# Optimization experiments

Measured on AMD Instinct MI355X. Metric: run time of the kernel, lower is better.

The kernel has to match this reference:

```python
import jax, jax.numpy as jnp
import numpy as np
from jax import lax

SUBSTEPS = 10
MACRO_DT = 1.0
MICRO_DT = MACRO_DT / float(SUBSTEPS)
MAX_DAYS = 4  # matches fill_max of delta_t_days; inactive batch items are masked to zero update


def _laplacian3d(u):
    # u: [B, 1, D, H, W]; 6-point stencil with zero (Dirichlet) padding at the boundary
    up = jnp.pad(u, ((0, 0), (0, 0), (1, 1), (1, 1), (1, 1)))
    return (up[:, :, 2:, 1:-1, 1:-1] + up[:, :, :-2, 1:-1, 1:-1]
            + up[:, :, 1:-1, 2:, 1:-1] + up[:, :, 1:-1, :-2, 1:-1]
            + up[:, :, 1:-1, 1:-1, 2:] + up[:, :, 1:-1, 1:-1, :-2]
            - 6.0 * u)


def _fisher_kolmogorov(u, D_map, rho_map):
    # du/dt = D * laplacian(u) + rho * u * (1 - u)
    return D_map * _laplacian3d(u) + rho_map * u * (1.0 - u)


def setup_inputs() -> dict:
    key = jax.random.key(0)
    k1, k2, k3, k4 = jax.random.split(key, 4)
    shape = (2, 1, 128, 128, 128)
    u_t0 = jax.random.uniform(k1, shape, dtype=jnp.float32)
    D_map = jax.random.uniform(k2, shape, dtype=jnp.float32) * 0.1   # diffusion, keep CFL-stable
    rho_map = jax.random.uniform(k3, shape, dtype=jnp.float32) * 0.5  # proliferation rate
    delta_t_days = jax.random.randint(k4, (2,), 0, MAX_DAYS, dtype=jnp.int32)
    return {"u_t0": u_t0, "D_map": D_map, "rho_map": rho_map, "delta_t_days": delta_t_days}


def reference(u_t0, D_map, rho_map, delta_t_days):
    # Sequential explicit-Euler rollout with per-batch-item active masking.
    days = jnp.arange(MAX_DAYS * SUBSTEPS, dtype=jnp.int32) // SUBSTEPS  # macro day of each micro-step

    def micro_step(u, day):
        active = (day < delta_t_days).astype(u.dtype)[:, None, None, None, None]  # [B,1,1,1,1]
        du_dt = _fisher_kolmogorov(u, D_map, rho_map)
        return u + active * MICRO_DT * du_dt, None

    u_final, _ = lax.scan(micro_step, u_t0, days)
    return jnp.clip(u_final, 0.0, 1.0)
```

## Files before the change

### kernel.cpp

```cpp
#include <hip/hip_runtime.h>
#include <cstdint>


constexpr int NX = 128, NY = 128, NZ = 128;
constexpr int PLANE = NX * NY;
constexpr int VOL   = NZ * PLANE;
constexpr int TOTAL = 2 * VOL;
constexpr float DT  = 0.1f;
constexpr int MAX_PAIRS = 20;

constexpr int TY = 8, TZ = 4;
constexpr int RY = TY + 2, RZ = TZ + 2;
constexpr int RING_ROWS = RZ * RY - TZ * TY;
constexpr int RING_F4   = RING_ROWS * 32;
constexpr int BLOCKS = 2 * (NZ / TZ) * (NY / TY);

__device__ __forceinline__ float4 ld4(const float* p) { return *(const float4*)p; }

__device__ __forceinline__ uint32_t f2bf(float f) {
    uint32_t u = __float_as_uint(f);
    u += 0x7fffu + ((u >> 16) & 1u);
    return u >> 16;
}
__device__ __forceinline__ float bf_lo(uint32_t p) { return __uint_as_float(p << 16); }
__device__ __forceinline__ float bf_hi(uint32_t p) { return __uint_as_float(p & 0xffff0000u); }
__device__ __forceinline__ float clip01(float v) { return fminf(fmaxf(v, 0.0f), 1.0f); }

__device__ __forceinline__ float4 fkstep(float4 c, float xm, float xp,
                                         float4 ym, float4 yp,
                                         float4 zm, float4 zp,
                                         float4 Dv, float4 Rv) {
    float4 o;
    o.x = fmaf(DT, fmaf(Dv.x, (xm + c.y) + (ym.x + yp.x) + (zm.x + zp.x) - 6.0f * c.x,
                        Rv.x * c.x * (1.0f - c.x)), c.x);
    o.y = fmaf(DT, fmaf(Dv.y, (c.x + c.z) + (ym.y + yp.y) + (zm.y + zp.y) - 6.0f * c.y,
                        Rv.y * c.y * (1.0f - c.y)), c.y);
    o.z = fmaf(DT, fmaf(Dv.z, (c.y + c.w) + (ym.z + yp.z) + (zm.z + zp.z) - 6.0f * c.z,
                        Rv.z * c.z * (1.0f - c.z)), c.z);
    o.w = fmaf(DT, fmaf(Dv.w, (c.z + xp) + (ym.w + yp.w) + (zm.w + zp.w) - 6.0f * c.w,
                        Rv.w * c.w * (1.0f - c.w)), c.w);
    return o;
}

__device__ __forceinline__ float4 unpackD(uint4 p) {
    return make_float4(bf_lo(p.x), bf_lo(p.y), bf_lo(p.z), bf_lo(p.w));
}
__device__ __forceinline__ float4 unpackR(uint4 p) {
    return make_float4(bf_hi(p.x), bf_hi(p.y), bf_hi(p.z), bf_hi(p.w));
}

__global__ __launch_bounds__(256, 4)
void fk_pair(const float* __restrict__ src, float* __restrict__ dst0,
             float* __restrict__ out, const float* __restrict__ u0,
             const float* __restrict__ Dm, const float* __restrict__ Rm,
             uint32_t* __restrict__ dr, const int* __restrict__ dtd, int p)
{
    const int b  = blockIdx.x >> 9;
    int d = dtd[b]; d = d < 0 ? 0 : (d > 4 ? 4 : d);
    const int steps = d * 10;

    const int zb = (blockIdx.x >> 4) & 31;
    const int yt = blockIdx.x & 15;
    const int z0 = zb * TZ, y0 = yt * TY;
    const int tid = threadIdx.x;
    const int xq  = tid & 31;
    const int yi  = tid >> 5;
    const int baseb = b << 21;
    const float4 zero = make_float4(0.f, 0.f, 0.f, 0.f);

    if (2 * p >= steps) {
        if (steps == 0 && p == 0) {
            #pragma unroll
            for (int k = 0; k < TZ; ++k) {
                const int idx = baseb + (z0 + k) * PLANE + (y0 + yi) * NX + (xq << 2);
                const float4 v = ld4(u0 + idx);
                float4 o;
                o.x = clip01(v.x); o.y = clip01(v.y);
                o.z = clip01(v.z); o.w = clip01(v.w);
                *(float4*)(out + idx) = o;
            }
        }
        return;
    }
    const bool first = (p == 0);
    const bool last  = (2 * p == steps - 2);
    float* __restrict__ dst = last ? out : dst0;

    __shared__ float s1[RZ * RY * NX];

    uint4 pr[TZ];
    {
        const int y = y0 + yi;
        const int colbase = baseb + y * NX + (xq << 2);
        const bool has_ym = (y > 0), has_yp = (y < NY - 1);
        const bool has_l = (xq > 0), has_r = (xq < 31);

        float4 um = (z0 > 0) ? ld4(src + colbase + (z0 - 1) * PLANE) : zero;
        float4 uc = ld4(src + colbase + z0 * PLANE);
        #pragma unroll
        for (int k = 0; k < TZ; ++k) {
            const int z = z0 + k;
            const int idx = colbase + z * PLANE;
            const float4 un = (z < NZ - 1) ? ld4(src + idx + PLANE) : zero;
            const float4 ym4 = has_ym ? ld4(src + idx - NX) : zero;
            const float4 yp4 = has_yp ? ld4(src + idx + NX) : zero;
            const float xm = has_l ? src[idx - 1] : 0.0f;
            const float xp = has_r ? src[idx + 4] : 0.0f;
            float4 Dv, Rv;
            if (first) {
                Dv = ld4(Dm + idx);
                Rv = ld4(Rm + idx);
                uint4 pk;
                pk.x = f2bf(Dv.x) | (f2bf(Rv.x) << 16);
                pk.y = f2bf(Dv.y) | (f2bf(Rv.y) << 16);
                pk.z = f2bf(Dv.z) | (f2bf(Rv.z) << 16);
                pk.w = f2bf(Dv.w) | (f2bf(Rv.w) << 16);
                *(uint4*)(dr + idx) = pk;
                pr[k] = pk;
            } else {
                pr[k] = *(const uint4*)(dr + idx);
                Dv = unpackD(pr[k]);
                Rv = unpackR(pr[k]);
            }
            const float4 o = fkstep(uc, xm, xp, ym4, yp4, um, un, Dv, Rv);
            *(float4*)&s1[((k + 1) * RY + (yi + 1)) * NX + (xq << 2)] = o;
            um = uc; uc = un;
        }
    }

    for (int i = tid; i < RING_F4; i += 256) {
        const int cxq = i & 31;
        const int r   = i >> 5;
        int rz, ry;
        if (r < 10)      { rz = 0; ry = r; }
        else if (r < 20) { rz = 5; ry = r - 10; }
        else { const int q = r - 20; rz = 1 + (q >> 1); ry = (q & 1) ? 9 : 0; }
        const int y = y0 - 1 + ry;
        const int z = z0 - 1 + rz;
        float4 o = zero;
        if ((unsigned)y < (unsigned)NY && (unsigned)z < (unsigned)NZ) {
            const int idx = baseb + z * PLANE + y * NX + (cxq << 2);
            const float4 c  = ld4(src + idx);
            const float xm  = (cxq > 0)  ? src[idx - 1] : 0.0f;
            const float xp  = (cxq < 31) ? src[idx + 4] : 0.0f;
            const float4 ym4 = (y > 0)      ? ld4(src + idx - NX)    : zero;
            const float4 yp4 = (y < NY - 1) ? ld4(src + idx + NX)    : zero;
            const float4 zm4 = (z > 0)      ? ld4(src + idx - PLANE) : zero;
            const float4 zp4 = (z < NZ - 1) ? ld4(src + idx + PLANE) : zero;
            float4 Dv, Rv;
            if (first) {
                Dv = ld4(Dm + idx);
                Rv = ld4(Rm + idx);
            } else {
                const uint4 pk = *(const uint4*)(dr + idx);
                Dv = unpackD(pk);
                Rv = unpackR(pk);
            }
            o = fkstep(c, xm, xp, ym4, yp4, zm4, zp4, Dv, Rv);
        }
        *(float4*)&s1[(rz * RY + ry) * NX + (cxq << 2)] = o;
    }
    __syncthreads();

    {
        const int ry = yi + 1;
        const int y  = y0 + yi;
        float4 zmv = *(const float4*)&s1[(0 * RY + ry) * NX + (xq << 2)];
        float4 cv  = *(const float4*)&s1[(1 * RY + ry) * NX + (xq << 2)];
        #pragma unroll
        for (int k = 0; k < TZ; ++k) {
            const int rz = k + 1;
            const float4 zpv = *(const float4*)&s1[((rz + 1) * RY + ry) * NX + (xq << 2)];
            const float* rowc = &s1[(rz * RY + ry) * NX];
            float xm = 0.0f, xp = 0.0f;
            if (xq > 0)  xm = ((const float4*)&rowc[(xq - 1) << 2])->w;
            if (xq < 31) xp = ((const float4*)&rowc[(xq + 1) << 2])->x;
            const float4 ym4 = *(const float4*)&s1[(rz * RY + ry - 1) * NX + (xq << 2)];
            const float4 yp4 = *(const float4*)&s1[(rz * RY + ry + 1) * NX + (xq << 2)];

            float4 o = fkstep(cv, xm, xp, ym4, yp4, zmv, zpv,
                              unpackD(pr[k]), unpackR(pr[k]));
            if (last) {
                o.x = clip01(o.x); o.y = clip01(o.y);
                o.z = clip01(o.z); o.w = clip01(o.w);
            }
            const int idx = baseb + (z0 + k) * PLANE + y * NX + (xq << 2);
            *(float4*)(dst + idx) = o;
            zmv = cv; cv = zpv;
        }
    }
}

extern "C" void kernel_launch(void* const* d_in, const int* in_sizes, int n_in,
                              void* d_out, int out_size, void* d_ws, size_t ws_size,
                              hipStream_t stream) {
    const float* u0  = (const float*)d_in[0];
    const float* Dm  = (const float*)d_in[1];
    const float* Rm  = (const float*)d_in[2];
    const int*   dtd = (const int*)d_in[3];
    float* out = (float*)d_out;
    float* ws  = (float*)d_ws;
    float* buf[2] = { ws, ws + TOTAL };
    uint32_t* dr = (uint32_t*)(ws + 2 * TOTAL);

    for (int p = 0; p < MAX_PAIRS; ++p) {
        const float* src = (p == 0) ? u0 : buf[(p - 1) & 1];
        fk_pair<<<BLOCKS, 256, 0, stream>>>(src, buf[p & 1], out, u0,
                                            Dm, Rm, dr, dtd, p);
    }
}
```

Measured before the change: 243.1 us.

## Fuse three Euler micro-steps per launch with two-level shared-memory halos

```diff
diff --git a/kernel.cpp b/kernel.cpp
--- a/kernel.cpp
+++ b/kernel.cpp
@@ -7,12 +7,11 @@
 constexpr int VOL   = NZ * PLANE;
 constexpr int TOTAL = 2 * VOL;
 constexpr float DT  = 0.1f;
-constexpr int MAX_PAIRS = 20;
+constexpr int MAX_TRIPLES = 10;
 
 constexpr int TY = 8, TZ = 4;
-constexpr int RY = TY + 2, RZ = TZ + 2;
-constexpr int RING_ROWS = RZ * RY - TZ * TY;
-constexpr int RING_F4   = RING_ROWS * 32;
+constexpr int S1Z = TZ + 4, S1Y = TY + 4;
+constexpr int S2Z = TZ + 2, S2Y = TY + 2;
 constexpr int BLOCKS = 2 * (NZ / TZ) * (NY / TY);
 
 __device__ __forceinline__ float4 ld4(const float* p) { return *(const float4*)p; }
@@ -26,18 +25,18 @@
 __device__ __forceinline__ float bf_hi(uint32_t p) { return __uint_as_float(p & 0xffff0000u); }
 __device__ __forceinline__ float clip01(float v) { return fminf(fmaxf(v, 0.0f), 1.0f); }
 
-__device__ __forceinline__ float4 fkstep(float4 c, float xm, float xp,
+__device__ __forceinline__ float4 fkstep(float dt, float4 c, float xm, float xp,
                                          float4 ym, float4 yp,
                                          float4 zm, float4 zp,
                                          float4 Dv, float4 Rv) {
     float4 o;
-    o.x = fmaf(DT, fmaf(Dv.x, (xm + c.y) + (ym.x + yp.x) + (zm.x + zp.x) - 6.0f * c.x,
+    o.x = fmaf(dt, fmaf(Dv.x, (xm + c.y) + (ym.x + yp.x) + (zm.x + zp.x) - 6.0f * c.x,
                         Rv.x * c.x * (1.0f - c.x)), c.x);
-    o.y = fmaf(DT, fmaf(Dv.y, (c.x + c.z) + (ym.y + yp.y) + (zm.y + zp.y) - 6.0f * c.y,
+    o.y = fmaf(dt, fmaf(Dv.y, (c.x + c.z) + (ym.y + yp.y) + (zm.y + zp.y) - 6.0f * c.y,
                         Rv.y * c.y * (1.0f - c.y)), c.y);
-    o.z = fmaf(DT, fmaf(Dv.z, (c.y + c.w) + (ym.z + yp.z) + (zm.z + zp.z) - 6.0f * c.z,
+    o.z = fmaf(dt, fmaf(Dv.z, (c.y + c.w) + (ym.z + yp.z) + (zm.z + zp.z) - 6.0f * c.z,
                         Rv.z * c.z * (1.0f - c.z)), c.z);
-    o.w = fmaf(DT, fmaf(Dv.w, (c.z + xp) + (ym.w + yp.w) + (zm.w + zp.w) - 6.0f * c.w,
+    o.w = fmaf(dt, fmaf(Dv.w, (c.z + xp) + (ym.w + yp.w) + (zm.w + zp.w) - 6.0f * c.w,
                         Rv.w * c.w * (1.0f - c.w)), c.w);
     return o;
 }
@@ -49,15 +48,16 @@
     return make_float4(bf_hi(p.x), bf_hi(p.y), bf_hi(p.z), bf_hi(p.w));
 }
 
-__global__ __launch_bounds__(256, 4)
-void fk_pair(const float* __restrict__ src, float* __restrict__ dst0,
-             float* __restrict__ out, const float* __restrict__ u0,
-             const float* __restrict__ Dm, const float* __restrict__ Rm,
-             uint32_t* __restrict__ dr, const int* __restrict__ dtd, int p)
+__global__ __launch_bounds__(256, 2)
+void fk_triple(const float* __restrict__ src, float* __restrict__ dst0,
+               float* __restrict__ out, const float* __restrict__ u0,
+               const float* __restrict__ Dm, const float* __restrict__ Rm,
+               uint32_t* __restrict__ dr, const int* __restrict__ dtd, int p)
 {
     const int b  = blockIdx.x >> 9;
-    int d = dtd[b]; d = d < 0 ? 0 : (d > 4 ? 4 : d);
+    int d = dtd[b]; d = d < 0 ? 0 : (d > 3 ? 3 : d);
     const int steps = d * 10;
+    const int g0 = 3 * p;
 
     const int zb = (blockIdx.x >> 4) & 31;
     const int yt = blockIdx.x & 15;
@@ -68,7 +68,7 @@
     const int baseb = b << 21;
     const float4 zero = make_float4(0.f, 0.f, 0.f, 0.f);
 
-    if (2 * p >= steps) {
+    if (g0 >= steps) {
         if (steps == 0 && p == 0) {
             #pragma unroll
             for (int k = 0; k < TZ; ++k) {
@@ -83,60 +83,70 @@
         return;
     }
     const bool first = (p == 0);
-    const bool last  = (2 * p == steps - 2);
+    const bool last  = (steps - g0 <= 3);
     float* __restrict__ dst = last ? out : dst0;
-
-    __shared__ float s1[RZ * RY * NX];
+    const float m1 = (g0 + 1 < steps) ? DT : 0.0f;
+    const float m2 = (g0 + 2 < steps) ? DT : 0.0f;
+
+    __shared__ float s1[S1Z * S1Y * NX];
+    __shared__ float s2[S2Z * S2Y * NX];
 
     uint4 pr[TZ];
+
     {
         const int y = y0 + yi;
         const int colbase = baseb + y * NX + (xq << 2);
         const bool has_ym = (y > 0), has_yp = (y < NY - 1);
         const bool has_l = (xq > 0), has_r = (xq < 31);
-
-        float4 um = (z0 > 0) ? ld4(src + colbase + (z0 - 1) * PLANE) : zero;
-        float4 uc = ld4(src + colbase + z0 * PLANE);
+        const int zlo = z0 - 2;
+
+        float4 um = ((unsigned)(zlo - 1) < (unsigned)NZ) ? ld4(src + colbase + (zlo - 1) * PLANE) : zero;
+        float4 uc = ((unsigned)zlo < (unsigned)NZ) ? ld4(src + colbase + zlo * PLANE) : zero;
         #pragma unroll
-        for (int k = 0; k < TZ; ++k) {
-            const int z = z0 + k;
+        for (int rz = 0; rz < S1Z; ++rz) {
+            const int z = zlo + rz;
             const int idx = colbase + z * PLANE;
-            const float4 un = (z < NZ - 1) ? ld4(src + idx + PLANE) : zero;
-            const float4 ym4 = has_ym ? ld4(src + idx - NX) : zero;
-            const float4 yp4 = has_yp ? ld4(src + idx + NX) : zero;
-            const float xm = has_l ? src[idx - 1] : 0.0f;
-            const float xp = has_r ? src[idx + 4] : 0.0f;
-            float4 Dv, Rv;
-            if (first) {
-                Dv = ld4(Dm + idx);
-                Rv = ld4(Rm + idx);
-                uint4 pk;
-                pk.x = f2bf(Dv.x) | (f2bf(Rv.x) << 16);
-                pk.y = f2bf(Dv.y) | (f2bf(Rv.y) << 16);
-                pk.z = f2bf(Dv.z) | (f2bf(Rv.z) << 16);
-                pk.w = f2bf(Dv.w) | (f2bf(Rv.w) << 16);
-                *(uint4*)(dr + idx) = pk;
-                pr[k] = pk;
-            } else {
-                pr[k] = *(const uint4*)(dr + idx);
-                Dv = unpackD(pr[k]);
-                Rv = unpackR(pr[k]);
-            }
-            const float4 o = fkstep(uc, xm, xp, ym4, yp4, um, un, Dv, Rv);
-            *(float4*)&s1[((k + 1) * RY + (yi + 1)) * NX + (xq << 2)] = o;
+            const float4 un = ((unsigned)(z + 1) < (unsigned)NZ) ? ld4(src + idx + PLANE) : zero;
+            float4 o = zero;
+            if ((unsigned)z < (unsigned)NZ) {
+                const float4 ym4 = has_ym ? ld4(src + idx - NX) : zero;
+                const float4 yp4 = has_yp ? ld4(src + idx + NX) : zero;
+                const float xm = has_l ? src[idx - 1] : 0.0f;
+                const float xp = has_r ? src[idx + 4] : 0.0f;
+                float4 Dv, Rv;
+                if (first) {
+                    Dv = ld4(Dm + idx);
+                    Rv = ld4(Rm + idx);
+                    if (rz >= 2 && rz < 2 + TZ) {
+                        uint4 pk;
+                        pk.x = f2bf(Dv.x) | (f2bf(Rv.x) << 16);
+                        pk.y = f2bf(Dv.y) | (f2bf(Rv.y) << 16);
+                        pk.z = f2bf(Dv.z) | (f2bf(Rv.z) << 16);
+                        pk.w = f2bf(Dv.w) | (f2bf(Rv.w) << 16);
+                        *(uint4*)(dr + idx) = pk;
+                        pr[rz - 2] = pk;
+                    }
+                } else {
+                    const uint4 pk = *(const uint4*)(dr + idx);
+                    Dv = unpackD(pk);
+                    Rv = unpackR(pk);
+                    if (rz >= 2 && rz < 2 + TZ) pr[rz - 2] = pk;
+                }
+                o = fkstep(DT, uc, xm, xp, ym4, yp4, um, un, Dv, Rv);
+            }
+            *(float4*)&s1[(rz * S1Y + (yi + 2)) * NX + (xq << 2)] = o;
             um = uc; uc = un;
         }
     }
 
-    for (int i = tid; i < RING_F4; i += 256) {
+    for (int i = tid; i < 32 * 32; i += 256) {
         const int cxq = i & 31;
         const int r   = i >> 5;
-        int rz, ry;
-        if (r < 10)      { rz = 0; ry = r; }
-        else if (r < 20) { rz = 5; ry = r - 10; }
-        else { const int q = r - 20; rz = 1 + (q >> 1); ry = (q & 1) ? 9 : 0; }
-        const int y = y0 - 1 + ry;
-        const int z = z0 - 1 + rz;
+        const int rr  = r >> 3;
+        const int rz  = r & 7;
+        const int ry  = (rr < 2) ? rr : rr + 8;
+        const int y = y0 - 2 + ry;
+        const int z = z0 - 2 + rz;
         float4 o = zero;
         if ((unsigned)y < (unsigned)NY && (unsigned)z < (unsigned)NZ) {
             const int idx = baseb + z * PLANE + y * NX + (cxq << 2);
@@ -156,29 +166,101 @@
                 Dv = unpackD(pk);
                 Rv = unpackR(pk);
             }
-            o = fkstep(c, xm, xp, ym4, yp4, zm4, zp4, Dv, Rv);
-        }
-        *(float4*)&s1[(rz * RY + ry) * NX + (cxq << 2)] = o;
+            o = fkstep(DT, c, xm, xp, ym4, yp4, zm4, zp4, Dv, Rv);
+        }
+        *(float4*)&s1[(rz * S1Y + ry) * NX + (cxq << 2)] = o;
     }
     __syncthreads();
 
     {
-        const int ry = yi + 1;
-        const int y  = y0 + yi;
-        float4 zmv = *(const float4*)&s1[(0 * RY + ry) * NX + (xq << 2)];
-        float4 cv  = *(const float4*)&s1[(1 * RY + ry) * NX + (xq << 2)];
+        const int ry2 = yi + 1;
+        const int ry1 = yi + 2;
+        float4 zmv = *(const float4*)&s1[(0 * S1Y + ry1) * NX + (xq << 2)];
+        float4 cv  = *(const float4*)&s1[(1 * S1Y + ry1) * NX + (xq << 2)];
+        #pragma unroll
+        for (int rz2 = 0; rz2 < S2Z; ++rz2) {
+            const int rz1 = rz2 + 1;
+            const float4 zpv = *(const float4*)&s1[((rz1 + 1) * S1Y + ry1) * NX + (xq << 2)];
+            const int z = z0 - 1 + rz2;
+            float4 o = zero;
+            if ((unsigned)z < (unsigned)NZ) {
+                const float* rowc = &s1[(rz1 * S1Y + ry1) * NX];
+                const float xm = (xq > 0)  ? rowc[(xq << 2) - 1] : 0.0f;
+                const float xp = (xq < 31) ? rowc[(xq << 2) + 4] : 0.0f;
+                const float4 ym4 = *(const float4*)&s1[(rz1 * S1Y + ry1 - 1) * NX + (xq << 2)];
+                const float4 yp4 = *(const float4*)&s1[(rz1 * S1Y + ry1 + 1) * NX + (xq << 2)];
+                float4 Dv, Rv;
+                if (rz2 >= 1 && rz2 < 1 + TZ) {
+                    Dv = unpackD(pr[rz2 - 1]);
+                    Rv = unpackR(pr[rz2 - 1]);
+                } else {
+                    const int idx = baseb + z * PLANE + (y0 + yi) * NX + (xq << 2);
+                    if (first) {
+                        Dv = ld4(Dm + idx);
+                        Rv = ld4(Rm + idx);
+                    } else {
+                        const uint4 pk = *(const uint4*)(dr + idx);
+                        Dv = unpackD(pk);
+                        Rv = unpackR(pk);
+                    }
+                }
+                o = fkstep(m1, cv, xm, xp, ym4, yp4, zmv, zpv, Dv, Rv);
+            }
+            *(float4*)&s2[(rz2 * S2Y + ry2) * NX + (xq << 2)] = o;
+            zmv = cv; cv = zpv;
+        }
+    }
+
+    for (int i = tid; i < 12 * 32; i += 256) {
+        const int cxq = i & 31;
+        const int r   = i >> 5;
+        const int ry2 = (r < 6) ? 0 : 9;
+        const int rz2 = (r < 6) ? r : r - 6;
+        const int y = y0 - 1 + ry2;
+        const int z = z0 - 1 + rz2;
+        float4 o = zero;
+        if ((unsigned)y < (unsigned)NY && (unsigned)z < (unsigned)NZ) {
+            const int rz1 = rz2 + 1, ry1 = ry2 + 1;
+            const float* rowc = &s1[(rz1 * S1Y + ry1) * NX];
+            const float4 cv = *(const float4*)&rowc[cxq << 2];
+            const float xm = (cxq > 0)  ? rowc[(cxq << 2) - 1] : 0.0f;
+            const float xp = (cxq < 31) ? rowc[(cxq << 2) + 4] : 0.0f;
+            const float4 ym4 = *(const float4*)&s1[(rz1 * S1Y + ry1 - 1) * NX + (cxq << 2)];
+            const float4 yp4 = *(const float4*)&s1[(rz1 * S1Y + ry1 + 1) * NX + (cxq << 2)];
+            const float4 zm4 = *(const float4*)&s1[((rz1 - 1) * S1Y + ry1) * NX + (cxq << 2)];
+            const float4 zp4 = *(const float4*)&s1[((rz1 + 1) * S1Y + ry1) * NX + (cxq << 2)];
+            float4 Dv, Rv;
+            const int idx = baseb + z * PLANE + y * NX + (cxq << 2);
+            if (first) {
+                Dv = ld4(Dm + idx);
+                Rv = ld4(Rm + idx);
+            } else {
+                const uint4 pk = *(const uint4*)(dr + idx);
+                Dv = unpackD(pk);
+                Rv = unpackR(pk);
+            }
+            o = fkstep(m1, cv, xm, xp, ym4, yp4, zm4, zp4, Dv, Rv);
+        }
+        *(float4*)&s2[(rz2 * S2Y + ry2) * NX + (cxq << 2)] = o;
+    }
+    __syncthreads();
+
+    {
+        const int ry2 = yi + 1;
+        const int y   = y0 + yi;
+        float4 zmv = *(const float4*)&s2[(0 * S2Y + ry2) * NX + (xq << 2)];
+        float4 cv  = *(const float4*)&s2[(1 * S2Y + ry2) * NX + (xq << 2)];
         #pragma unroll
         for (int k = 0; k < TZ; ++k) {
-            const int rz = k + 1;
-            const float4 zpv = *(const float4*)&s1[((rz + 1) * RY + ry) * NX + (xq << 2)];
-            const float* rowc = &s1[(rz * RY + ry) * NX];
-            float xm = 0.0f, xp = 0.0f;
-            if (xq > 0)  xm = ((const float4*)&rowc[(xq - 1) << 2])->w;
-            if (xq < 31) xp = ((const float4*)&rowc[(xq + 1) << 2])->x;
-            const float4 ym4 = *(const float4*)&s1[(rz * RY + ry - 1) * NX + (xq << 2)];
-            const float4 yp4 = *(const float4*)&s1[(rz * RY + ry + 1) * NX + (xq << 2)];
-
-            float4 o = fkstep(cv, xm, xp, ym4, yp4, zmv, zpv,
+            const int rz2 = k + 1;
+            const float4 zpv = *(const float4*)&s2[((rz2 + 1) * S2Y + ry2) * NX + (xq << 2)];
+            const float* rowc = &s2[(rz2 * S2Y + ry2) * NX];
+            const float xm = (xq > 0)  ? rowc[(xq << 2) - 1] : 0.0f;
+            const float xp = (xq < 31) ? rowc[(xq << 2) + 4] : 0.0f;
+            const float4 ym4 = *(const float4*)&s2[(rz2 * S2Y + ry2 - 1) * NX + (xq << 2)];
+            const float4 yp4 = *(const float4*)&s2[(rz2 * S2Y + ry2 + 1) * NX + (xq << 2)];
+
+            float4 o = fkstep(m2, cv, xm, xp, ym4, yp4, zmv, zpv,
                               unpackD(pr[k]), unpackR(pr[k]));
             if (last) {
                 o.x = clip01(o.x); o.y = clip01(o.y);
@@ -203,9 +285,9 @@
     float* buf[2] = { ws, ws + TOTAL };
     uint32_t* dr = (uint32_t*)(ws + 2 * TOTAL);
 
-    for (int p = 0; p < MAX_PAIRS; ++p) {
+    for (int p = 0; p < MAX_TRIPLES; ++p) {
         const float* src = (p == 0) ? u0 : buf[(p - 1) & 1];
-        fk_pair<<<BLOCKS, 256, 0, stream>>>(src, buf[p & 1], out, u0,
-                                            Dm, Rm, dr, dtd, p);
-    }
-}
+        fk_triple<<<BLOCKS, 256, 0, stream>>>(src, buf[p & 1], out, u0,
+                                              Dm, Rm, dr, dtd, p);
+    }
+}
```

After: 232.8 us. -4.3%, faster.

## Fuse three Euler substeps per launch with shared-memory temporal blocking

Applied to the files above, without the earlier changes.

```diff
diff --git a/kernel.cpp b/kernel.cpp
--- a/kernel.cpp
+++ b/kernel.cpp
@@ -7,12 +7,9 @@
 constexpr int VOL   = NZ * PLANE;
 constexpr int TOTAL = 2 * VOL;
 constexpr float DT  = 0.1f;
-constexpr int MAX_PAIRS = 20;
-
-constexpr int TY = 8, TZ = 4;
-constexpr int RY = TY + 2, RZ = TZ + 2;
-constexpr int RING_ROWS = RZ * RY - TZ * TY;
-constexpr int RING_F4   = RING_ROWS * 32;
+constexpr int MAX_TRIPLES = 10;
+
+constexpr int TY = 4, TZ = 4;
 constexpr int BLOCKS = 2 * (NZ / TZ) * (NY / TY);
 
 __device__ __forceinline__ float4 ld4(const float* p) { return *(const float4*)p; }
@@ -26,18 +23,18 @@
 __device__ __forceinline__ float bf_hi(uint32_t p) { return __uint_as_float(p & 0xffff0000u); }
 __device__ __forceinline__ float clip01(float v) { return fminf(fmaxf(v, 0.0f), 1.0f); }
 
-__device__ __forceinline__ float4 fkstep(float4 c, float xm, float xp,
+__device__ __forceinline__ float4 fkstep(float dt, float4 c, float xm, float xp,
                                          float4 ym, float4 yp,
                                          float4 zm, float4 zp,
                                          float4 Dv, float4 Rv) {
     float4 o;
-    o.x = fmaf(DT, fmaf(Dv.x, (xm + c.y) + (ym.x + yp.x) + (zm.x + zp.x) - 6.0f * c.x,
+    o.x = fmaf(dt, fmaf(Dv.x, (xm + c.y) + (ym.x + yp.x) + (zm.x + zp.x) - 6.0f * c.x,
                         Rv.x * c.x * (1.0f - c.x)), c.x);
-    o.y = fmaf(DT, fmaf(Dv.y, (c.x + c.z) + (ym.y + yp.y) + (zm.y + zp.y) - 6.0f * c.y,
+    o.y = fmaf(dt, fmaf(Dv.y, (c.x + c.z) + (ym.y + yp.y) + (zm.y + zp.y) - 6.0f * c.y,
                         Rv.y * c.y * (1.0f - c.y)), c.y);
-    o.z = fmaf(DT, fmaf(Dv.z, (c.y + c.w) + (ym.z + yp.z) + (zm.z + zp.z) - 6.0f * c.z,
+    o.z = fmaf(dt, fmaf(Dv.z, (c.y + c.w) + (ym.z + yp.z) + (zm.z + zp.z) - 6.0f * c.z,
                         Rv.z * c.z * (1.0f - c.z)), c.z);
-    o.w = fmaf(DT, fmaf(Dv.w, (c.z + xp) + (ym.w + yp.w) + (zm.w + zp.w) - 6.0f * c.w,
+    o.w = fmaf(dt, fmaf(Dv.w, (c.z + xp) + (ym.w + yp.w) + (zm.w + zp.w) - 6.0f * c.w,
                         Rv.w * c.w * (1.0f - c.w)), c.w);
     return o;
 }
@@ -50,29 +47,34 @@
 }
 
 __global__ __launch_bounds__(256, 4)
-void fk_pair(const float* __restrict__ src, float* __restrict__ dst0,
-             float* __restrict__ out, const float* __restrict__ u0,
-             const float* __restrict__ Dm, const float* __restrict__ Rm,
-             uint32_t* __restrict__ dr, const int* __restrict__ dtd, int p)
+void fk_triple(const float* __restrict__ src, float* __restrict__ dst0,
+               float* __restrict__ out, const float* __restrict__ u0,
+               const float* __restrict__ Dm, const float* __restrict__ Rm,
+               uint32_t* __restrict__ dr, const int* __restrict__ dtd, int p)
 {
-    const int b  = blockIdx.x >> 9;
-    int d = dtd[b]; d = d < 0 ? 0 : (d > 4 ? 4 : d);
+    const int b  = blockIdx.x >> 10;
+    int d = dtd[b]; d = d < 0 ? 0 : (d > 3 ? 3 : d);
     const int steps = d * 10;
-
-    const int zb = (blockIdx.x >> 4) & 31;
-    const int yt = blockIdx.x & 15;
+    const int g0 = 3 * p;
+
+    const int zb = (blockIdx.x >> 5) & 31;
+    const int yt = blockIdx.x & 31;
     const int z0 = zb * TZ, y0 = yt * TY;
     const int tid = threadIdx.x;
-    const int xq  = tid & 31;
-    const int yi  = tid >> 5;
+    const int cxq = tid & 31;
+    const int ry  = tid >> 5;
     const int baseb = b << 21;
     const float4 zero = make_float4(0.f, 0.f, 0.f, 0.f);
 
-    if (2 * p >= steps) {
+    if (g0 >= steps) {
         if (steps == 0 && p == 0) {
             #pragma unroll
-            for (int k = 0; k < TZ; ++k) {
-                const int idx = baseb + (z0 + k) * PLANE + (y0 + yi) * NX + (xq << 2);
+            for (int kk = 0; kk < 2; ++kk) {
+                const int t  = tid + kk * 256;
+                const int zk = t >> 7;
+                const int yy = (t >> 5) & 3;
+                const int cq = t & 31;
+                const int idx = baseb + (z0 + zk) * PLANE + (y0 + yy) * NX + (cq << 2);
                 const float4 v = ld4(u0 + idx);
                 float4 o;
                 o.x = clip01(v.x); o.y = clip01(v.y);
@@ -83,70 +85,107 @@
         return;
     }
     const bool first = (p == 0);
-    const bool last  = (2 * p == steps - 2);
+    const bool last  = (steps - g0 <= 3);
     float* __restrict__ dst = last ? out : dst0;
-
-    __shared__ float s1[RZ * RY * NX];
-
-    uint4 pr[TZ];
-    {
-        const int y = y0 + yi;
-        const int colbase = baseb + y * NX + (xq << 2);
-        const bool has_ym = (y > 0), has_yp = (y < NY - 1);
-        const bool has_l = (xq > 0), has_r = (xq < 31);
-
-        float4 um = (z0 > 0) ? ld4(src + colbase + (z0 - 1) * PLANE) : zero;
-        float4 uc = ld4(src + colbase + z0 * PLANE);
-        #pragma unroll
-        for (int k = 0; k < TZ; ++k) {
-            const int z = z0 + k;
-            const int idx = colbase + z * PLANE;
-            const float4 un = (z < NZ - 1) ? ld4(src + idx + PLANE) : zero;
-            const float4 ym4 = has_ym ? ld4(src + idx - NX) : zero;
-            const float4 yp4 = has_yp ? ld4(src + idx + NX) : zero;
-            const float xm = has_l ? src[idx - 1] : 0.0f;
-            const float xp = has_r ? src[idx + 4] : 0.0f;
+    const float m1 = (g0 + 1 < steps) ? DT : 0.0f;
+    const float m2 = (g0 + 2 < steps) ? DT : 0.0f;
+
+    __shared__ float r1[3][8][NX];
+    __shared__ float r2[3][6][NX];
+
+    const int  yA = y0 - 2 + ry;
+    const bool vy = (unsigned)yA < (unsigned)NY;
+    const int  colA = baseb + yA * NX + (cxq << 2);
+    const bool hl = (cxq > 0), hr = (cxq < 31);
+
+    float4 um = zero, uc = zero;
+    if (vy) {
+        if (z0 - 3 >= 0) um = ld4(src + colA + (z0 - 3) * PLANE);
+        if (z0 - 2 >= 0) uc = ld4(src + colA + (z0 - 2) * PLANE);
+    }
+
+    #pragma unroll
+    for (int i = 0; i < 8; ++i) {
+        const int z1 = z0 - 2 + i;
+
+        float4 un = zero;
+        if (vy && (unsigned)(z1 + 1) < (unsigned)NZ)
+            un = ld4(src + colA + (z1 + 1) * PLANE);
+        float4 o1 = zero;
+        if (vy && (unsigned)z1 < (unsigned)NZ) {
+            const int idx = colA + z1 * PLANE;
+            const float4 ym4 = (yA > 0)      ? ld4(src + idx - NX) : zero;
+            const float4 yp4 = (yA < NY - 1) ? ld4(src + idx + NX) : zero;
+            const float xm = hl ? src[idx - 1] : 0.0f;
+            const float xp = hr ? src[idx + 4] : 0.0f;
             float4 Dv, Rv;
             if (first) {
                 Dv = ld4(Dm + idx);
                 Rv = ld4(Rm + idx);
-                uint4 pk;
-                pk.x = f2bf(Dv.x) | (f2bf(Rv.x) << 16);
-                pk.y = f2bf(Dv.y) | (f2bf(Rv.y) << 16);
-                pk.z = f2bf(Dv.z) | (f2bf(Rv.z) << 16);
-                pk.w = f2bf(Dv.w) | (f2bf(Rv.w) << 16);
-                *(uint4*)(dr + idx) = pk;
-                pr[k] = pk;
+                if (ry >= 2 && ry < 6 && i >= 2 && i < 6) {
+                    uint4 pk;
+                    pk.x = f2bf(Dv.x) | (f2bf(Rv.x) << 16);
+                    pk.y = f2bf(Dv.y) | (f2bf(Rv.y) << 16);
+                    pk.z = f2bf(Dv.z) | (f2bf(Rv.z) << 16);
+                    pk.w = f2bf(Dv.w) | (f2bf(Rv.w) << 16);
+                    *(uint4*)(dr + idx) = pk;
+                }
             } else {
-                pr[k] = *(const uint4*)(dr + idx);
-                Dv = unpackD(pr[k]);
-                Rv = unpackR(pr[k]);
-            }
-            const float4 o = fkstep(uc, xm, xp, ym4, yp4, um, un, Dv, Rv);
-            *(float4*)&s1[((k + 1) * RY + (yi + 1)) * NX + (xq << 2)] = o;
-            um = uc; uc = un;
-        }
-    }
-
-    for (int i = tid; i < RING_F4; i += 256) {
-        const int cxq = i & 31;
-        const int r   = i >> 5;
-        int rz, ry;
-        if (r < 10)      { rz = 0; ry = r; }
-        else if (r < 20) { rz = 5; ry = r - 10; }
-        else { const int q = r - 20; rz = 1 + (q >> 1); ry = (q & 1) ? 9 : 0; }
-        const int y = y0 - 1 + ry;
-        const int z = z0 - 1 + rz;
-        float4 o = zero;
-        if ((unsigned)y < (unsigned)NY && (unsigned)z < (unsigned)NZ) {
-            const int idx = baseb + z * PLANE + y * NX + (cxq << 2);
-            const float4 c  = ld4(src + idx);
-            const float xm  = (cxq > 0)  ? src[idx - 1] : 0.0f;
-            const float xp  = (cxq < 31) ? src[idx + 4] : 0.0f;
-            const float4 ym4 = (y > 0)      ? ld4(src + idx - NX)    : zero;
-            const float4 yp4 = (y < NY - 1) ? ld4(src + idx + NX)    : zero;
-            const float4 zm4 = (z > 0)      ? ld4(src + idx - PLANE) : zero;
-            const float4 zp4 = (z < NZ - 1) ? ld4(src + idx + PLANE) : zero;
+                const uint4 pk = *(const uint4*)(dr + idx);
+                Dv = unpackD(pk);
+                Rv = unpackR(pk);
+            }
+            o1 = fkstep(DT, uc, xm, xp, ym4, yp4, um, un, Dv, Rv);
+        }
+        *(float4*)&r1[i % 3][ry][cxq << 2] = o1;
+        um = uc; uc = un;
+        __syncthreads();
+
+        if (i >= 2) {
+            const int z2 = z1 - 1;
+            if (ry < 6) {
+                float4 o2 = zero;
+                const int yB = y0 - 1 + ry;
+                if ((unsigned)z2 < (unsigned)NZ && (unsigned)yB < (unsigned)NY) {
+                    const int sm = (i - 2) % 3, sc = (i - 1) % 3, sp = i % 3;
+                    const float* rowc = &r1[sc][ry + 1][0];
+                    const float4 cc  = *(const float4*)&rowc[cxq << 2];
+                    const float xm = hl ? rowc[(cxq << 2) - 1] : 0.0f;
+                    const float xp = hr ? rowc[(cxq << 2) + 4] : 0.0f;
+                    const float4 ym4 = *(const float4*)&r1[sc][ry][cxq << 2];
+                    const float4 yp4 = *(const float4*)&r1[sc][ry + 2][cxq << 2];
+                    const float4 zm4 = *(const float4*)&r1[sm][ry + 1][cxq << 2];
+                    const float4 zp4 = *(const float4*)&r1[sp][ry + 1][cxq << 2];
+                    const int idx = baseb + z2 * PLANE + yB * NX + (cxq << 2);
+                    float4 Dv, Rv;
+                    if (first) {
+                        Dv = ld4(Dm + idx);
+                        Rv = ld4(Rm + idx);
+                    } else {
+                        const uint4 pk = *(const uint4*)(dr + idx);
+                        Dv = unpackD(pk);
+                        Rv = unpackR(pk);
+                    }
+                    o2 = fkstep(m1, cc, xm, xp, ym4, yp4, zm4, zp4, Dv, Rv);
+                }
+                *(float4*)&r2[(i - 2) % 3][ry][cxq << 2] = o2;
+            }
+        }
+        __syncthreads();
+
+        if (i >= 4 && ry < 4) {
+            const int zo = z0 - 4 + i;
+            const int yC = y0 + ry;
+            const int qm = (i - 4) % 3, qc = (i - 3) % 3, qp = (i - 2) % 3;
+            const float* rowc = &r2[qc][ry + 1][0];
+            const float4 cc  = *(const float4*)&rowc[cxq << 2];
+            const float xm = hl ? rowc[(cxq << 2) - 1] : 0.0f;
+            const float xp = hr ? rowc[(cxq << 2) + 4] : 0.0f;
+            const float4 ym4 = *(const float4*)&r2[qc][ry][cxq << 2];
+            const float4 yp4 = *(const float4*)&r2[qc][ry + 2][cxq << 2];
+            const float4 zm4 = *(const float4*)&r2[qm][ry + 1][cxq << 2];
+            const float4 zp4 = *(const float4*)&r2[qp][ry + 1][cxq << 2];
+            const int idx = baseb + zo * PLANE + yC * NX + (cxq << 2);
             float4 Dv, Rv;
             if (first) {
                 Dv = ld4(Dm + idx);
@@ -156,37 +195,12 @@
                 Dv = unpackD(pk);
                 Rv = unpackR(pk);
             }
-            o = fkstep(c, xm, xp, ym4, yp4, zm4, zp4, Dv, Rv);
-        }
-        *(float4*)&s1[(rz * RY + ry) * NX + (cxq << 2)] = o;
-    }
-    __syncthreads();
-
-    {
-        const int ry = yi + 1;
-        const int y  = y0 + yi;
-        float4 zmv = *(const float4*)&s1[(0 * RY + ry) * NX + (xq << 2)];
-        float4 cv  = *(const float4*)&s1[(1 * RY + ry) * NX + (xq << 2)];
-        #pragma unroll
-        for (int k = 0; k < TZ; ++k) {
-            const int rz = k + 1;
-            const float4 zpv = *(const float4*)&s1[((rz + 1) * RY + ry) * NX + (xq << 2)];
-            const float* rowc = &s1[(rz * RY + ry) * NX];
-            float xm = 0.0f, xp = 0.0f;
-            if (xq > 0)  xm = ((const float4*)&rowc[(xq - 1) << 2])->w;
-            if (xq < 31) xp = ((const float4*)&rowc[(xq + 1) << 2])->x;
-            const float4 ym4 = *(const float4*)&s1[(rz * RY + ry - 1) * NX + (xq << 2)];
-            const float4 yp4 = *(const float4*)&s1[(rz * RY + ry + 1) * NX + (xq << 2)];
-
-            float4 o = fkstep(cv, xm, xp, ym4, yp4, zmv, zpv,
-                              unpackD(pr[k]), unpackR(pr[k]));
+            float4 o3 = fkstep(m2, cc, xm, xp, ym4, yp4, zm4, zp4, Dv, Rv);
             if (last) {
-                o.x = clip01(o.x); o.y = clip01(o.y);
-                o.z = clip01(o.z); o.w = clip01(o.w);
-            }
-            const int idx = baseb + (z0 + k) * PLANE + y * NX + (xq << 2);
-            *(float4*)(dst + idx) = o;
-            zmv = cv; cv = zpv;
+                o3.x = clip01(o3.x); o3.y = clip01(o3.y);
+                o3.z = clip01(o3.z); o3.w = clip01(o3.w);
+            }
+            *(float4*)(dst + idx) = o3;
         }
     }
 }
@@ -203,9 +217,9 @@
     float* buf[2] = { ws, ws + TOTAL };
     uint32_t* dr = (uint32_t*)(ws + 2 * TOTAL);
 
-    for (int p = 0; p < MAX_PAIRS; ++p) {
+    for (int p = 0; p < MAX_TRIPLES; ++p) {
         const float* src = (p == 0) ? u0 : buf[(p - 1) & 1];
-        fk_pair<<<BLOCKS, 256, 0, stream>>>(src, buf[p & 1], out, u0,
-                                            Dm, Rm, dr, dtd, p);
-    }
-}
+        fk_triple<<<BLOCKS, 256, 0, stream>>>(src, buf[p & 1], out, u0,
+                                              Dm, Rm, dr, dtd, p);
+    }
+}
```

New measurement: 277.2 us. +14.0%, slower.
